# Kernel optimization log

Measured on AMD Instinct MI355X. Metric: run time of the kernel, lower is better.

## Reference

```python
import jax, jax.numpy as jnp
import numpy as np

EPS = 1e-08


def setup_inputs() -> dict:
    key = jax.random.key(0)
    k1, k2 = jax.random.split(key)
    z = jax.random.normal(k1, (32, 768, 32, 32), dtype=jnp.float32)
    memory = jax.random.normal(k2, (512, 768), dtype=jnp.float32)
    return {"z": z, "memory": memory}


def _l2_normalize(x, axis=-1, eps=1e-12):
    # Matches torch F.normalize(dim=-1): x / max(||x||, eps)
    n = jnp.sqrt(jnp.sum(x * x, axis=axis, keepdims=True))
    return x / jnp.maximum(n, eps)


def reference(z, memory):
    B, C, H, W = z.shape
    M = memory.shape[0]
    # (B, C, H, W) -> (B, H*W, C)
    z_flat = jnp.transpose(z, (0, 2, 3, 1)).reshape(B, H * W, C)
    z_norm = _l2_normalize(z_flat)
    mem_norm = _l2_normalize(memory)
    # cosine-similarity scores: (B, N, M)
    scores = jnp.einsum('bnc,mc->bnm', z_norm, mem_norm)
    w = jax.nn.softmax(scores, axis=-1)
    lam = 1.0 / M
    # hard-shrink sparsification: relu(w - lam) * w / (|w - lam| + eps)
    d = w - lam
    attn_w = jax.nn.relu(d) * w / (jnp.abs(d) + EPS)
    attn_w = attn_w / (jnp.sum(attn_w, axis=-1, keepdims=True) + EPS)
    # weighted readout against the RAW (un-normalized) memory
    z_hat_flat = jnp.einsum('bnm,mc->bnc', attn_w, memory)
    z_hat = jnp.transpose(z_hat_flat.reshape(B, H, W, C), (0, 3, 1, 2))
    return (z_hat, attn_w)
```

## Files before the change

kernel.cpp:

```cpp
#include <hip/hip_runtime.h>
#include <hip/hip_bf16.h>
#include <math.h>

typedef short short8 __attribute__((ext_vector_type(8)));
typedef float f32x4 __attribute__((ext_vector_type(4)));
typedef _Float16 f16x8 __attribute__((ext_vector_type(8)));

#define CC 768
#define NN 1024
#define RR 32768
#define MM 512
#define ZSTRIDE 786432
#define OUT_ATTN_OFF 25165824
#define SPLIT_SC 2048.0f
#define INV_SC   (1.0f / 2048.0f)

static __device__ __forceinline__ short f2bf(float f) {
    __hip_bfloat16 h = __float2bfloat16(f);
    return *reinterpret_cast<short*>(&h);
}

static __device__ __forceinline__ double fast_exp_neg(double x) {
    const double LOG2E = 1.4426950408889634074;
    const double LN2   = 0.6931471805599453094;
    const double MAGIC = 6755399441055744.0;
    double t = x * LOG2E;
    double c = t + MAGIC;
    double n = c - MAGIC;
    int ni = (int)__double2loint(c);
    double g = (t - n) * LN2;
    double r = 2.505210838544172e-08;
    r = fma(r, g, 2.755731922398589e-07);
    r = fma(r, g, 2.7557319223985893e-06);
    r = fma(r, g, 2.48015873015873e-05);
    r = fma(r, g, 1.984126984126984e-04);
    r = fma(r, g, 1.388888888888889e-03);
    r = fma(r, g, 8.333333333333333e-03);
    r = fma(r, g, 4.1666666666666664e-02);
    r = fma(r, g, 1.6666666666666666e-01);
    r = fma(r, g, 0.5);
    r = fma(r, g, 1.0);
    r = fma(r, g, 1.0);
    double sc = __hiloint2double((1023 + ni) << 20, 0);
    return r * sc;
}

static __device__ __forceinline__ double fast_rcp(double x) {
    double r = (double)(1.0f / (float)x);
    r = r * (2.0 - x * r);
    r = r * (2.0 - x * r);
    return r;
}

__global__ __launch_bounds__(256) void prep_mem_kernel(const float* __restrict__ memory,
                                                       _Float16* __restrict__ mem_h,
                                                       _Float16* __restrict__ mem_L,
                                                       short* __restrict__ memT_bf) {
    int m = blockIdx.x;
    int t = threadIdx.x;
    double ss = 0.0;
    for (int c = t; c < CC; c += 256) {
        float v = memory[m * CC + c];
        ss += (double)v * (double)v;
    }
    #pragma unroll
    for (int off = 32; off > 0; off >>= 1) ss += __shfl_xor(ss, off);
    __shared__ double red[4];
    __shared__ double invs;
    if ((t & 63) == 0) red[t >> 6] = ss;
    __syncthreads();
    if (t == 0) {
        double tot = red[0] + red[1] + red[2] + red[3];
        invs = 1.0 / fmax(sqrt(tot), 1e-12);
    }
    __syncthreads();
    float inv = (float)invs;
    for (int c = t; c < CC; c += 256) {
        float v  = memory[m * CC + c];
        float nv = v * inv;
        _Float16 h = (_Float16)nv;
        float r1 = nv - (float)h;
        mem_h[m * CC + c] = h;
        mem_L[m * CC + c] = (_Float16)(r1 * SPLIT_SC);
        memT_bf[c * MM + m] = f2bf(v);
    }
}

#define SWZ(row_, k_) ((((row_) << 5) + (k_)) ^ (((row_) & 7) << 3))
__global__ __launch_bounds__(512, 4) void scores_gemm_kernel(const float* __restrict__ z,
                                                             const _Float16* __restrict__ mem_h,
                                                             const _Float16* __restrict__ mem_L,
                                                             float* __restrict__ out_scores,
                                                             double* __restrict__ zinv_ws) {
    __shared__ _Float16 AT[2][2][4096];
    __shared__ _Float16 BT[2][2][4096];
    __shared__ double ssred[512];

    const int t    = threadIdx.x;
    const int lane = t & 63;
    const int wv   = t >> 6;
    const int lrow = lane & 15;
    const int gk   = lane >> 4;
    const int wr   = wv >> 1, wc = wv & 1;
    const int d = blockIdx.x;
    const int colblk = (d >> 3) & 3;
    const int rowblk = (d & 7) | ((d >> 5) << 3);
    const int row0 = rowblk * 128;
    const int b    = row0 >> 10;
    const int n0   = row0 & 1023;
    const int cB0  = colblk * 128;

    const int an  = t & 127;
    const int ak8 = (t >> 7) * 8;
    const float* zA = z + (size_t)b * ZSTRIDE + n0 + an;

    const int br0 = ((t >> 2) ^ (t >> 4)) & 1;
    const int br  = ((t >> 3) << 1) | br0;
    const int bk8 = (((t & 3) ^ ((((t >> 3) & 1) << 1) | br0)) << 3);
    const _Float16* srcBh = mem_h + (size_t)(cB0 + br) * CC + bk8;
    const _Float16* srcBL = mem_L + (size_t)(cB0 + br) * CC + bk8;

    double ss = 0.0;
    f32x4 am[2][4], ax[2][4];
    #pragma unroll
    for (int fc = 0; fc < 2; ++fc)
        #pragma unroll
        for (int fn = 0; fn < 4; ++fn) {
            am[fc][fn] = (f32x4){0.f, 0.f, 0.f, 0.f};
            ax[fc][fn] = (f32x4){0.f, 0.f, 0.f, 0.f};
        }

    float avX[8], avY[8];

    #define DMA_B(bb_, kt_)                                                    \
        do {                                                                   \
            __builtin_amdgcn_global_load_lds(                                  \
                (const __attribute__((address_space(1))) void*)(srcBh + (kt_) * 32), \
                (__attribute__((address_space(3))) void*)(&BT[bb_][0][wv * 512]),    \
                16, 0, 0);                                                     \
            __builtin_amdgcn_global_load_lds(                                  \
                (const __attribute__((address_space(1))) void*)(srcBL + (kt_) * 32), \
                (__attribute__((address_space(3))) void*)(&BT[bb_][1][wv * 512]),    \
                16, 0, 0);                                                     \
        } while (0)

    #define LOAD_A(kt_, av_)                                                   \
        do {                                                                   \
            _Pragma("unroll")                                                  \
            for (int j = 0; j < 8; ++j)                                        \
                av_[j] = zA[(size_t)((kt_) * 32 + ak8 + j) * NN];              \
        } while (0)

    #define WRITE_A(bb_, av_)                                                  \
        do {                                                                   \
            f16x8 h8, l8;                                                      \
            _Pragma("unroll")                                                  \
            for (int j = 0; j < 8; ++j) {                                      \
                float v = av_[j];                                              \
                ss = fma((double)v, (double)v, ss);                            \
                _Float16 h = (_Float16)v;                                      \
                h8[j] = h;                                                     \
                l8[j] = (_Float16)((v - (float)h) * SPLIT_SC);                 \
            }                                                                  \
            *reinterpret_cast<f16x8*>(&AT[bb_][0][SWZ(an, ak8)]) = h8;         \
            *reinterpret_cast<f16x8*>(&AT[bb_][1][SWZ(an, ak8)]) = l8;         \
        } while (0)

    #define MFMA_BLOCK(cur_)                                                       \
        do {                                                                       \
            f16x8 ah0 = *reinterpret_cast<const f16x8*>(                           \
                &AT[cur_][0][SWZ(wr * 32 + lrow, gk * 8)]);                        \
            f16x8 ah1 = *reinterpret_cast<const f16x8*>(                           \
                &AT[cur_][0][SWZ(wr * 32 + 16 + lrow, gk * 8)]);                   \
            f16x8 aL0 = *reinterpret_cast<const f16x8*>(                           \
                &AT[cur_][1][SWZ(wr * 32 + lrow, gk * 8)]);                        \
            f16x8 aL1 = *reinterpret_cast<const f16x8*>(                           \
                &AT[cur_][1][SWZ(wr * 32 + 16 + lrow, gk * 8)]);                   \
            _Pragma("unroll")                                                      \
            for (int fn = 0; fn < 4; ++fn) {                                       \
                f16x8 bhf = *reinterpret_cast<const f16x8*>(                       \
                    &BT[cur_][0][SWZ(wc * 64 + fn * 16 + lrow, gk * 8)]);          \
                f16x8 bLf = *reinterpret_cast<const f16x8*>(                       \
                    &BT[cur_][1][SWZ(wc * 64 + fn * 16 + lrow, gk * 8)]);          \
                am[0][fn] = __builtin_amdgcn_mfma_f32_16x16x32_f16(ah0, bhf, am[0][fn], 0, 0, 0); \
                ax[0][fn] = __builtin_amdgcn_mfma_f32_16x16x32_f16(aL0, bhf, ax[0][fn], 0, 0, 0); \
                ax[0][fn] = __builtin_amdgcn_mfma_f32_16x16x32_f16(ah0, bLf, ax[0][fn], 0, 0, 0); \
                am[1][fn] = __builtin_amdgcn_mfma_f32_16x16x32_f16(ah1, bhf, am[1][fn], 0, 0, 0); \
                ax[1][fn] = __builtin_amdgcn_mfma_f32_16x16x32_f16(aL1, bhf, ax[1][fn], 0, 0, 0); \
                ax[1][fn] = __builtin_amdgcn_mfma_f32_16x16x32_f16(ah1, bLf, ax[1][fn], 0, 0, 0); \
            }                                                                      \
        } while (0)

    DMA_B(0, 0);
    LOAD_A(0, avX);
    WRITE_A(0, avX);
    LOAD_A(1, avY);
    __syncthreads();

    #pragma unroll 1
    for (int kt = 0; kt < 24; kt += 2) {
        if (kt + 1 < 24) DMA_B(1, kt + 1);
        if (kt + 2 < 24) LOAD_A(kt + 2, avX);
        MFMA_BLOCK(0);
        if (kt + 1 < 24) WRITE_A(1, avY);
        __syncthreads();
        if (kt + 2 < 24) DMA_B(0, kt + 2);
        if (kt + 3 < 24) LOAD_A(kt + 3, avY);
        MFMA_BLOCK(1);
        if (kt + 2 < 24) WRITE_A(0, avX);
        __syncthreads();
    }
    #undef DMA_B
    #undef LOAD_A
    #undef WRITE_A
    #undef MFMA_BLOCK

    #pragma unroll
    for (int fc = 0; fc < 2; ++fc)
        #pragma unroll
        for (int fn = 0; fn < 4; ++fn)
            #pragma unroll
            for (int rg = 0; rg < 4; ++rg) {
                int row = row0 + wr * 32 + fc * 16 + gk * 4 + rg;
                int col = cB0 + wc * 64 + fn * 16 + lrow;
                out_scores[(size_t)row * MM + col] = am[fc][fn][rg] + ax[fc][fn][rg] * INV_SC;
            }

    ssred[t] = ss;
    __syncthreads();
    if (colblk == 0 && t < 128) {
        double tot = ssred[t] + ssred[t + 128] + ssred[t + 256] + ssred[t + 384];
        zinv_ws[row0 + t] = 1.0 / fmax(sqrt(tot), 1e-12);
    }
}
#undef SWZ

__global__ __launch_bounds__(256) void epilogue_kernel(float* __restrict__ attn,
                                                       const double* __restrict__ zinv_ws) {
    const int t    = threadIdx.x;
    const int lane = t & 63;
    const int wv   = t >> 6;
    const int row0 = blockIdx.x * 64;

    #pragma unroll 1
    for (int i = 0; i < 16; ++i) {
        int row = row0 + wv * 16 + i;
        double zi = zinv_ws[row];
        float* rp = attn + (size_t)row * MM;
        f32x4 x0 = *reinterpret_cast<const f32x4*>(&rp[lane * 4]);
        f32x4 x1 = *reinterpret_cast<const f32x4*>(&rp[256 + lane * 4]);
        double s0 = (double)x0[0] * zi, s1 = (double)x0[1] * zi;
        double s2 = (double)x0[2] * zi, s3 = (double)x0[3] * zi;
        double s4 = (double)x1[0] * zi, s5 = (double)x1[1] * zi;
        double s6 = (double)x1[2] * zi, s7 = (double)x1[3] * zi;
        double mx = fmax(fmax(fmax(s0, s1), fmax(s2, s3)),
                         fmax(fmax(s4, s5), fmax(s6, s7)));
        #pragma unroll
        for (int off = 32; off > 0; off >>= 1) mx = fmax(mx, __shfl_xor(mx, off));
        double p0 = fast_exp_neg(s0 - mx), p1 = fast_exp_neg(s1 - mx);
        double p2 = fast_exp_neg(s2 - mx), p3 = fast_exp_neg(s3 - mx);
        double p4 = fast_exp_neg(s4 - mx), p5 = fast_exp_neg(s5 - mx);
        double p6 = fast_exp_neg(s6 - mx), p7 = fast_exp_neg(s7 - mx);
        double Z = ((p0 + p1) + (p2 + p3)) + ((p4 + p5) + (p6 + p7));
        #pragma unroll
        for (int off = 32; off > 0; off >>= 1) Z += __shfl_xor(Z, off);
        double iZ = fast_rcp(Z);
        const double LAM = 1.0 / 512.0;
        double w0 = p0 * iZ, w1 = p1 * iZ, w2 = p2 * iZ, w3 = p3 * iZ;
        double w4 = p4 * iZ, w5 = p5 * iZ, w6 = p6 * iZ, w7 = p7 * iZ;
        double d0 = w0 - LAM, d1 = w1 - LAM, d2 = w2 - LAM, d3 = w3 - LAM;
        double d4 = w4 - LAM, d5 = w5 - LAM, d6 = w6 - LAM, d7 = w7 - LAM;
        double e0 = (d0 > 0.0 ? d0 : 0.0) * w0 * fast_rcp(fabs(d0) + 1e-8);
        double e1 = (d1 > 0.0 ? d1 : 0.0) * w1 * fast_rcp(fabs(d1) + 1e-8);
        double e2 = (d2 > 0.0 ? d2 : 0.0) * w2 * fast_rcp(fabs(d2) + 1e-8);
        double e3 = (d3 > 0.0 ? d3 : 0.0) * w3 * fast_rcp(fabs(d3) + 1e-8);
        double e4 = (d4 > 0.0 ? d4 : 0.0) * w4 * fast_rcp(fabs(d4) + 1e-8);
        double e5 = (d5 > 0.0 ? d5 : 0.0) * w5 * fast_rcp(fabs(d5) + 1e-8);
        double e6 = (d6 > 0.0 ? d6 : 0.0) * w6 * fast_rcp(fabs(d6) + 1e-8);
        double e7 = (d7 > 0.0 ? d7 : 0.0) * w7 * fast_rcp(fabs(d7) + 1e-8);
        double S = ((e0 + e1) + (e2 + e3)) + ((e4 + e5) + (e6 + e7));
        #pragma unroll
        for (int off = 32; off > 0; off >>= 1) S += __shfl_xor(S, off);
        double rinv = fast_rcp(S + 1e-8);
        f32x4 o0 = { (float)(e0 * rinv), (float)(e1 * rinv),
                     (float)(e2 * rinv), (float)(e3 * rinv) };
        f32x4 o1 = { (float)(e4 * rinv), (float)(e5 * rinv),
                     (float)(e6 * rinv), (float)(e7 * rinv) };
        *reinterpret_cast<f32x4*>(&rp[lane * 4])       = o0;
        *reinterpret_cast<f32x4*>(&rp[256 + lane * 4]) = o1;
    }
}

__global__ __launch_bounds__(256, 3) void readout_kernel(const short* __restrict__ memT_bf,
                                                         const float* __restrict__ attn,
                                                         float* __restrict__ out) {
    __shared__ short At[128][40];
    __shared__ short Bt[128][40];
    const int t = threadIdx.x;
    const int d  = blockIdx.x;
    const int xs = d & 7;
    const int hi = d >> 3;
    const int c0idx  = hi % 6;
    const int rowmid = hi / 6;
    const int rb     = xs | (rowmid << 3);
    const int c0     = c0idx * 128;
    const int rowblk = rb * 128;
    const int b  = rowblk >> 10;
    const int nb = rowblk & 1023;
    const int lane = t & 63, wv = t >> 6;
    const int wcr = wv >> 1, wcc = wv & 1;
    const int lrow = lane & 15, gk = lane >> 4;

    f32x4 acc[4][4];
    #pragma unroll
    for (int fc = 0; fc < 4; ++fc)
        #pragma unroll
        for (int fn = 0; fn < 4; ++fn) acc[fc][fn] = (f32x4){0.f, 0.f, 0.f, 0.f};

    const int sr = t >> 1;
    const int ko = (t & 1) * 16;

    for (int m0 = 0; m0 < MM; m0 += 32) {
        __syncthreads();
        {
            const short8* src = reinterpret_cast<const short8*>(
                &memT_bf[(c0 + sr) * MM + m0 + ko]);
            *reinterpret_cast<short8*>(&At[sr][ko])     = src[0];
            *reinterpret_cast<short8*>(&At[sr][ko + 8]) = src[1];
        }
        {
            const f32x4* src = reinterpret_cast<const f32x4*>(
                &attn[(size_t)(rowblk + sr) * MM + m0 + ko]);
            f32x4 v0 = src[0], v1 = src[1], v2 = src[2], v3 = src[3];
            short8 s0 = { f2bf(v0[0]), f2bf(v0[1]), f2bf(v0[2]), f2bf(v0[3]),
                          f2bf(v1[0]), f2bf(v1[1]), f2bf(v1[2]), f2bf(v1[3]) };
            short8 s1 = { f2bf(v2[0]), f2bf(v2[1]), f2bf(v2[2]), f2bf(v2[3]),
                          f2bf(v3[0]), f2bf(v3[1]), f2bf(v3[2]), f2bf(v3[3]) };
            *reinterpret_cast<short8*>(&Bt[sr][ko])     = s0;
            *reinterpret_cast<short8*>(&Bt[sr][ko + 8]) = s1;
        }
        __syncthreads();
        short8 af[4], bf[4];
        #pragma unroll
        for (int fc = 0; fc < 4; ++fc)
            af[fc] = *reinterpret_cast<const short8*>(&At[wcr * 64 + fc * 16 + lrow][gk * 8]);
        #pragma unroll
        for (int fn = 0; fn < 4; ++fn)
            bf[fn] = *reinterpret_cast<const short8*>(&Bt[wcc * 64 + fn * 16 + lrow][gk * 8]);
        #pragma unroll
        for (int fc = 0; fc < 4; ++fc)
            #pragma unroll
            for (int fn = 0; fn < 4; ++fn)
                acc[fc][fn] = __builtin_amdgcn_mfma_f32_16x16x32_bf16(af[fc], bf[fn], acc[fc][fn], 0, 0, 0);
    }

    #pragma unroll
    for (int fc = 0; fc < 4; ++fc)
        #pragma unroll
        for (int fn = 0; fn < 4; ++fn)
            #pragma unroll
            for (int reg = 0; reg < 4; ++reg) {
                int c = c0 + wcr * 64 + fc * 16 + gk * 4 + reg;
                int n = nb + wcc * 64 + fn * 16 + lrow;
                out[(size_t)b * ZSTRIDE + (size_t)c * NN + n] = acc[fc][fn][reg];
            }
}

extern "C" void kernel_launch(void* const* d_in, const int* in_sizes, int n_in,
                              void* d_out, int out_size, void* d_ws, size_t ws_size,
                              hipStream_t stream) {
    const float* z      = (const float*)d_in[0];
    const float* memory = (const float*)d_in[1];
    float* out      = (float*)d_out;
    float* out_attn = out + OUT_ATTN_OFF;

    char* wsb = (char*)d_ws;
    _Float16* mem_h   = (_Float16*)wsb;
    _Float16* mem_L   = (_Float16*)(wsb + 786432);
    short*    memT_bf = (short*)(wsb + 1572864);
    double*   zinv_ws = (double*)(wsb + 2359296);

    prep_mem_kernel<<<512, 256, 0, stream>>>(memory, mem_h, mem_L, memT_bf);
    scores_gemm_kernel<<<1024, 512, 0, stream>>>(z, mem_h, mem_L, out_attn, zinv_ws);
    epilogue_kernel<<<RR / 64, 256, 0, stream>>>(out_attn, zinv_ws);
    readout_kernel<<<1536, 256, 0, stream>>>(memT_bf, out_attn, out);
}
```

Baseline: 192.2 us.

## Double-buffer readout GEMM with async global-to-LDS loads and swizzled LDS

Reworks the readout kernel's K loop into a double-buffered pipeline. The memory tile is fetched straight into LDS with global_load_lds, the next attention tile is loaded into registers while the current tile's MFMAs run, and one barrier per step replaces two. Padded LDS arrays become XOR-swizzled flat buffers to avoid bank conflicts. This hides global-load latency behind compute, at the cost of doubled shared memory and more intricate index math that could cut occupancy.

```diff
diff --git a/kernel.cpp b/kernel.cpp
--- a/kernel.cpp
+++ b/kernel.cpp
@@ -233,7 +233,6 @@
         zinv_ws[row0 + t] = 1.0 / fmax(sqrt(tot), 1e-12);
     }
 }
-#undef SWZ
 
 __global__ __launch_bounds__(256) void epilogue_kernel(float* __restrict__ attn,
                                                        const double* __restrict__ zinv_ws) {
@@ -294,8 +293,8 @@
 __global__ __launch_bounds__(256, 3) void readout_kernel(const short* __restrict__ memT_bf,
                                                          const float* __restrict__ attn,
                                                          float* __restrict__ out) {
-    __shared__ short At[128][40];
-    __shared__ short Bt[128][40];
+    __shared__ short At[2][4096];
+    __shared__ short Bt[2][4096];
     const int t = threadIdx.x;
     const int d  = blockIdx.x;
     const int xs = d & 7;
@@ -317,42 +316,94 @@
         #pragma unroll
         for (int fn = 0; fn < 4; ++fn) acc[fc][fn] = (f32x4){0.f, 0.f, 0.f, 0.f};
 
+    int ar[2], ak[2];
+    #pragma unroll
+    for (int i = 0; i < 2; ++i) {
+        int u = i * 256 + t;
+        int r0 = ((u >> 2) ^ (u >> 4)) & 1;
+        ar[i] = ((u >> 3) << 1) | r0;
+        ak[i] = ((u & 3) ^ ((((u >> 3) & 1) << 1) | r0)) << 3;
+    }
     const int sr = t >> 1;
     const int ko = (t & 1) * 16;
-
-    for (int m0 = 0; m0 < MM; m0 += 32) {
+    const float* attnB = attn + (size_t)(rowblk + sr) * MM + ko;
+
+    #define RSWZ(row_, k_) ((((row_) << 5) + (k_)) ^ (((row_) & 7) << 3))
+
+    #define DMA_A(bb_, m0_)                                                    \
+        do {                                                                   \
+            __builtin_amdgcn_global_load_lds(                                  \
+                (const __attribute__((address_space(1))) void*)                \
+                    (memT_bf + (size_t)(c0 + ar[0]) * MM + (m0_) + ak[0]),     \
+                (__attribute__((address_space(3))) void*)(&At[bb_][wv * 512]), \
+                16, 0, 0);                                                     \
+            __builtin_amdgcn_global_load_lds(                                  \
+                (const __attribute__((address_space(1))) void*)                \
+                    (memT_bf + (size_t)(c0 + ar[1]) * MM + (m0_) + ak[1]),     \
+                (__attribute__((address_space(3))) void*)(&At[bb_][2048 + wv * 512]), \
+                16, 0, 0);                                                     \
+        } while (0)
+
+    #define LOAD_B(m0_, v_)                                                    \
+        do {                                                                   \
+            const f32x4* src = reinterpret_cast<const f32x4*>(attnB + (m0_));  \
+            v_[0] = src[0]; v_[1] = src[1]; v_[2] = src[2]; v_[3] = src[3];    \
+        } while (0)
+
+    #define WRITE_B(bb_, v_)                                                   \
+        do {                                                                   \
+            short8 s0 = { f2bf(v_[0][0]), f2bf(v_[0][1]), f2bf(v_[0][2]), f2bf(v_[0][3]), \
+                          f2bf(v_[1][0]), f2bf(v_[1][1]), f2bf(v_[1][2]), f2bf(v_[1][3]) }; \
+            short8 s1 = { f2bf(v_[2][0]), f2bf(v_[2][1]), f2bf(v_[2][2]), f2bf(v_[2][3]), \
+                          f2bf(v_[3][0]), f2bf(v_[3][1]), f2bf(v_[3][2]), f2bf(v_[3][3]) }; \
+            *reinterpret_cast<short8*>(&Bt[bb_][RSWZ(sr, ko)])     = s0;       \
+            *reinterpret_cast<short8*>(&Bt[bb_][RSWZ(sr, ko + 8)]) = s1;       \
+        } while (0)
+
+    #define MFMA_STEP(bb_)                                                     \
+        do {                                                                   \
+            short8 af[4], bf[4];                                               \
+            _Pragma("unroll")                                                  \
+            for (int fc = 0; fc < 4; ++fc)                                     \
+                af[fc] = *reinterpret_cast<const short8*>(                     \
+                    &At[bb_][RSWZ(wcr * 64 + fc * 16 + lrow, gk * 8)]);        \
+            _Pragma("unroll")                                                  \
+            for (int fn = 0; fn < 4; ++fn)                                     \
+                bf[fn] = *reinterpret_cast<const short8*>(                     \
+                    &Bt[bb_][RSWZ(wcc * 64 + fn * 16 + lrow, gk * 8)]);        \
+            _Pragma("unroll")                                                  \
+            for (int fc = 0; fc < 4; ++fc)                                     \
+                _Pragma("unroll")                                              \
+                for (int fn = 0; fn < 4; ++fn)                                 \
+                    acc[fc][fn] = __builtin_amdgcn_mfma_f32_16x16x32_bf16(     \
+                        af[fc], bf[fn], acc[fc][fn], 0, 0, 0);                 \
+        } while (0)
+
+    {
+        f32x4 v[4];
+        DMA_A(0, 0);
+        LOAD_B(0, v);
+        WRITE_B(0, v);
+    }
+    __syncthreads();
+
+    #pragma unroll 1
+    for (int step = 0; step < 16; ++step) {
+        const int cur = step & 1;
+        f32x4 v[4];
+        if (step < 15) {
+            DMA_A(cur ^ 1, (step + 1) * 32);
+            LOAD_B((step + 1) * 32, v);
+        }
+        MFMA_STEP(cur);
+        if (step < 15) WRITE_B(cur ^ 1, v);
         __syncthreads();
-        {
-            const short8* src = reinterpret_cast<const short8*>(
-                &memT_bf[(c0 + sr) * MM + m0 + ko]);
-            *reinterpret_cast<short8*>(&At[sr][ko])     = src[0];
-            *reinterpret_cast<short8*>(&At[sr][ko + 8]) = src[1];
-        }
-        {
-            const f32x4* src = reinterpret_cast<const f32x4*>(
-                &attn[(size_t)(rowblk + sr) * MM + m0 + ko]);
-            f32x4 v0 = src[0], v1 = src[1], v2 = src[2], v3 = src[3];
-            short8 s0 = { f2bf(v0[0]), f2bf(v0[1]), f2bf(v0[2]), f2bf(v0[3]),
-                          f2bf(v1[0]), f2bf(v1[1]), f2bf(v1[2]), f2bf(v1[3]) };
-            short8 s1 = { f2bf(v2[0]), f2bf(v2[1]), f2bf(v2[2]), f2bf(v2[3]),
-                          f2bf(v3[0]), f2bf(v3[1]), f2bf(v3[2]), f2bf(v3[3]) };
-            *reinterpret_cast<short8*>(&Bt[sr][ko])     = s0;
-            *reinterpret_cast<short8*>(&Bt[sr][ko + 8]) = s1;
-        }
-        __syncthreads();
-        short8 af[4], bf[4];
-        #pragma unroll
-        for (int fc = 0; fc < 4; ++fc)
-            af[fc] = *reinterpret_cast<const short8*>(&At[wcr * 64 + fc * 16 + lrow][gk * 8]);
-        #pragma unroll
-        for (int fn = 0; fn < 4; ++fn)
-            bf[fn] = *reinterpret_cast<const short8*>(&Bt[wcc * 64 + fn * 16 + lrow][gk * 8]);
-        #pragma unroll
-        for (int fc = 0; fc < 4; ++fc)
-            #pragma unroll
-            for (int fn = 0; fn < 4; ++fn)
-                acc[fc][fn] = __builtin_amdgcn_mfma_f32_16x16x32_bf16(af[fc], bf[fn], acc[fc][fn], 0, 0, 0);
-    }
+    }
+    #undef DMA_A
+    #undef LOAD_B
+    #undef WRITE_B
+    #undef MFMA_STEP
+    #undef RSWZ
 
     #pragma unroll
     for (int fc = 0; fc < 4; ++fc)
@@ -365,6 +416,7 @@
                 out[(size_t)b * ZSTRIDE + (size_t)c * NN + n] = acc[fc][fn][reg];
             }
 }
+#undef SWZ
 
 extern "C" void kernel_launch(void* const* d_in, const int* in_sizes, int n_in,
                               void* d_out, int out_size, void* d_ws, size_t ws_size,
```

Result: no change. 190.6 us (-0.8%).
